# Kernel optimization log

Measured on AMD Instinct MI355X. Metric: run time of the kernel, lower is better.

## Reference

```python
import jax, jax.numpy as jnp
import numpy as np

N, E, IN, HID, H, OUT = 50000, 800000, 128, 64, 2, 1
NEG_SLOPE = 0.2


def setup_inputs() -> dict:
    key = jax.random.key(0)
    ks = jax.random.split(key, 12)
    g = lambda k, shape, fi, fo: jax.random.normal(k, shape, jnp.float32) * np.sqrt(2.0 / (fi + fo)).astype(np.float32)
    x = jax.random.normal(ks[0], (N, IN), jnp.float32)
    edge_index = jax.random.randint(ks[1], (2, E), 0, N, jnp.int64)
    HC = H * HID
    W1 = g(ks[2], (HC, IN), IN, HC)
    b1 = jnp.zeros((HC,), jnp.float32)
    att1 = g(ks[3], (1, H, HID), HID, HID)
    W2 = g(ks[4], (HC, HC), HC, HC)
    b2 = jnp.zeros((HC,), jnp.float32)
    att2 = g(ks[5], (1, H, HID), HID, HID)
    Wp1 = g(ks[6], (HID, HC), HC, HID)
    bp1 = jnp.zeros((HID,), jnp.float32)
    Wp2 = g(ks[7], (OUT, HID), HID, OUT)
    bp2 = jnp.zeros((OUT,), jnp.float32)
    return {"x": x, "edge_index": edge_index, "W1": W1, "b1": b1, "att1": att1,
            "W2": W2, "b2": b2, "att2": att2, "Wp1": Wp1, "bp1": bp1, "Wp2": Wp2, "bp2": bp2}


def _segment_softmax(alpha, idx, n):
    # alpha: [E, H]; softmax over edges sharing the same destination node
    m = jax.ops.segment_max(alpha, idx, num_segments=n)
    m = jnp.where(jnp.isfinite(m), m, 0.0)  # empty segments -> -inf guard
    ex = jnp.exp(alpha - m[idx])
    s = jax.ops.segment_sum(ex, idx, num_segments=n)
    return ex / (s[idx] + 1e-16)


def _gatv2(x, edge_index, W, b, att):
    n = x.shape[0]
    h, c = att.shape[1], att.shape[2]
    xw = (x @ W.T + b).reshape(n, h, c)          # shared lin_l == lin_r
    src, dst = edge_index[0], edge_index[1]       # x_j = xw[src], x_i = xw[dst]
    xj = xw[src]                                  # [E, H, C]
    e = jax.nn.leaky_relu(xw[dst] + xj, NEG_SLOPE)
    alpha = jnp.einsum('ehc,ohc->eh', e, att)     # [E, H]
    alpha = _segment_softmax(alpha, dst, n)
    msg = xj * alpha[:, :, None]                  # message uses x_j (not e)
    out = jax.ops.segment_sum(msg, dst, num_segments=n)
    return out.reshape(n, h * c)


def reference(x, edge_index, W1, b1, att1, W2, b2, att2, Wp1, bp1, Wp2, bp2):
    # eval mode: dropout is identity
    h = jax.nn.relu(_gatv2(x, edge_index, W1, b1, att1))
    h = jax.nn.relu(_gatv2(h, edge_index, W2, b2, att2))
    h = h @ Wp1.T + bp1
    h = h @ Wp2.T + bp2
    return jax.nn.sigmoid(h)
```

## Files before the change

kernel.cpp:

```cpp
#include <hip/hip_runtime.h>
#include <math.h>

typedef __attribute__((ext_vector_type(2))) float f32x2;
typedef __attribute__((ext_vector_type(4))) float fx4;
typedef __attribute__((ext_vector_type(8))) short s16x8;

#define EC 64
#define NRR 8
#define RRN 6250


__device__ __forceinline__ unsigned pack_bf2(float lo, float hi){
  unsigned ul = __float_as_uint(lo); ul += 0x7fffu + ((ul>>16)&1u);
  unsigned uh = __float_as_uint(hi); uh += 0x7fffu + ((uh>>16)&1u);
  return (uh & 0xffff0000u) | (ul >> 16);
}


__device__ __forceinline__ void gemm_core(uint4* Wl, const float* __restrict__ X,
    const float* __restrict__ b, unsigned short* __restrict__ Ybf, int nrows, int brow, int t)
{
  int wv = t >> 6, lane = t & 63;
  int r = lane & 15, kb = lane >> 4;
  int row = brow*64 + wv*16 + r;
  const float* xrow = &X[(size_t)min(row, nrows-1)*128];

  fx4 acc[8];
  #pragma unroll
  for(int c=0;c<8;c++) acc[c] = (fx4){0.f,0.f,0.f,0.f};

  #pragma unroll
  for(int kt=0;kt<4;kt++){
    int k0 = kt*32 + kb*8;
    float4 v0 = *(const float4*)&xrow[k0];
    float4 v1 = *(const float4*)&xrow[k0+4];
    float vs[8] = {v0.x,v0.y,v0.z,v0.w,v1.x,v1.y,v1.z,v1.w};
    s16x8 ahi, alo;
    #pragma unroll
    for(int j=0;j<8;j++){
      unsigned u = __float_as_uint(vs[j]);
      unsigned uh = u + 0x7fffu + ((u>>16)&1u);
      unsigned short h = (unsigned short)(uh >> 16);
      float hf = __uint_as_float(((unsigned)h)<<16);
      float lo = vs[j] - hf;
      unsigned ul = __float_as_uint(lo);
      ul += 0x7fffu + ((ul>>16)&1u);
      ahi[j] = (short)h;
      alo[j] = (short)(ul>>16);
    }
    int chunk = kt*4 + kb;
    #pragma unroll
    for(int c=0;c<8;c++){
      uint4 wb = Wl[((c*16 + r)<<4) | (chunk ^ r)];
      s16x8 bb = *(s16x8*)&wb;
      acc[c] = __builtin_amdgcn_mfma_f32_16x16x32_bf16(ahi, bb, acc[c], 0,0,0);
      acc[c] = __builtin_amdgcn_mfma_f32_16x16x32_bf16(alo, bb, acc[c], 0,0,0);
    }
  }

  __syncthreads();
  unsigned short* lds = (unsigned short*)Wl;
  unsigned short* my = lds + wv*2048;
  int colb = lane & 15;
  int rq0 = (lane>>4)*4;
  #pragma unroll
  for(int c=0;c<8;c++){
    int col = c*16 + colb;
    float bias = b[col];
    #pragma unroll
    for(int q=0;q<4;q++){
      unsigned u = __float_as_uint(acc[c][q] + bias);
      u += 0x7fffu + ((u>>16)&1u);
      my[(rq0+q)*128 + col] = (unsigned short)(u>>16);
    }
  }
  const uint4* my4 = (const uint4*)my;
  uint4* Y4 = (uint4*)Ybf;
  #pragma unroll
  for(int rr=0;rr<4;rr++){
    int idx = lane + 64*rr;
    int lrow = idx >> 4, lcol = idx & 15;
    int grow = brow*64 + wv*16 + lrow;
    if(grow < nrows)
      Y4[(size_t)grow*16 + lcol] = my4[idx];
  }
}


__global__ __launch_bounds__(256) void mega_k(
    const float* __restrict__ X, const float* __restrict__ W1, const float* __restrict__ b1,
    unsigned short* __restrict__ XWbf, int nrows, int nGB,
    const int* __restrict__ dst, int E, int CH,
    unsigned short* __restrict__ cnt16, int N,
    const float* __restrict__ W2, unsigned short* __restrict__ W2bf,
    const float* __restrict__ Wp1, const float* __restrict__ bp1,
    const float* __restrict__ Wp2, const float* __restrict__ bp2,
    float* __restrict__ wfold)
{
  __shared__ int smem[8192];
  int b = blockIdx.x;
  int t = threadIdx.x;

  if(b < nGB){
    uint4* Wl = (uint4*)smem;
    #pragma unroll
    for(int i=0;i<8;i++){
      int idx = t + i*256;
      int row = idx >> 4, ch = idx & 15;
      const float* wsrc = &W1[(size_t)row*128 + ch*8];
      float4 va = *(const float4*)&wsrc[0];
      float4 vb = *(const float4*)&wsrc[4];
      uint4 o;
      o.x = pack_bf2(va.x, va.y); o.y = pack_bf2(va.z, va.w);
      o.z = pack_bf2(vb.x, vb.y); o.w = pack_bf2(vb.z, vb.w);
      Wl[(row<<4) | (ch ^ (row & 15))] = o;
    }
    __syncthreads();
    gemm_core(Wl, X, b1, XWbf, nrows, b, t);
    return;
  }
  int hb = b - nGB;
  if(hb < NRR*EC){
    int r = hb >> 6, c = hb & (EC-1);
    int r0 = r*RRN, rend = min(r0+RRN, N);
    int rn = rend - r0;
    if(rn <= 0) return;
    for(int d=t; d<rn; d+=256) smem[d] = 0;
    __syncthreads();
    int e0 = c*CH, e1 = min(e0+CH, E);
    for(int e = e0+t; e < e1; e += 256){
      int d = dst[e];
      if(d >= r0 && d < rend) atomicAdd(&smem[d-r0], 1);
    }
    __syncthreads();
    unsigned short* outp = cnt16 + (size_t)c*N;
    for(int d=t; d<rn; d+=256) outp[r0+d] = (unsigned short)smem[d];
    return;
  }
  int tb = hb - NRR*EC;
  if(tb == 0){
    const float4* Ws = (const float4*)W2;
    uint2* Wd = (uint2*)W2bf;
    #pragma unroll
    for(int i=0;i<16;i++){
      int idx = t + i*256;
      float4 v = Ws[idx];
      uint2 o; o.x = pack_bf2(v.x, v.y); o.y = pack_bf2(v.z, v.w);
      Wd[idx] = o;
    }
    return;
  }
  int k = t;
  if(k < 128){
    float s = 0.f;
    for(int j=0;j<64;j++) s += Wp2[j]*Wp1[(size_t)j*128 + k];
    wfold[k] = s;
  } else if(k == 128){
    float s = bp2[0];
    for(int j=0;j<64;j++) s += Wp2[j]*bp1[j];
    wfold[128] = s;
  }
}


__global__ __launch_bounds__(1024) void scan1_k(const unsigned short* __restrict__ cnt16,
    unsigned short* __restrict__ offs16, int* __restrict__ total,
    int* __restrict__ bsum, int n){
  __shared__ int ws[16];
  int i = blockIdx.x*1024 + threadIdx.x;
  int v = 0;
  if(i < n){
    int s = 0;
    #pragma unroll
    for(int c=0;c<EC;c++){
      int tc = cnt16[(size_t)c*n + i];
      offs16[(size_t)c*n + i] = (unsigned short)s;
      s += tc;
    }
    total[i] = s;
    v = s;
  }
  #pragma unroll
  for(int m=1;m<64;m<<=1) v += __shfl_xor(v, m);
  if((threadIdx.x & 63) == 0) ws[threadIdx.x >> 6] = v;
  __syncthreads();
  if(threadIdx.x == 0){
    int s = 0;
    #pragma unroll
    for(int w=0; w<16; w++) s += ws[w];
    bsum[blockIdx.x] = s;
  }
}


__global__ __launch_bounds__(1024) void scan3_k(const int* __restrict__ total,
    const int* __restrict__ bsum, int nb, int* __restrict__ row_ptr, int n){
  __shared__ int sm[1024];
  __shared__ int base_s;
  int t = threadIdx.x;
  if(t < 64){
    int bv = (t < nb && t < (int)blockIdx.x) ? bsum[t] : 0;
    #pragma unroll
    for(int m=1;m<64;m<<=1) bv += __shfl_xor(bv, m);
    if(t == 0) base_s = bv;
  }
  int i = blockIdx.x*1024 + t;
  int v = (i<n)? total[i] : 0;
  sm[t] = v;
  __syncthreads();
  for(int off=1; off<1024; off<<=1){
    int tv = (t>=off)? sm[t-off] : 0;
    __syncthreads();
    sm[t] += tv;
    __syncthreads();
  }
  if(i<n){
    row_ptr[i] = sm[t] - v + base_s;
    if(i == n-1) row_ptr[n] = sm[t] + base_s;
  }
}


__global__ __launch_bounds__(256) void fillC_k(
    const int* __restrict__ src, const int* __restrict__ dst,
    const unsigned short* __restrict__ offs16, const int* __restrict__ row_ptr,
    int* __restrict__ csr_src, int E, int CH, int N)
{
  __shared__ int cursor[RRN];
  int b = blockIdx.x, t = threadIdx.x;
  int r = b >> 6, c = b & (EC-1);
  int r0 = r*RRN, rend = min(r0+RRN, N);
  int rn = rend - r0;
  if(rn <= 0) return;
  for(int d=t; d<rn; d+=256)
    cursor[d] = row_ptr[r0+d] + (int)offs16[(size_t)c*N + r0 + d];
  __syncthreads();
  int e0 = c*CH, e1 = min(e0+CH, E);
  for(int base = e0 + t; base < e1; base += 1024){
    int ea = base, eb = base+256, ec2 = base+512, ed = base+768;
    int da = dst[ea];
    int db = (eb < e1) ? dst[eb] : -1;
    int dc = (ec2 < e1) ? dst[ec2] : -1;
    int dd = (ed < e1) ? dst[ed] : -1;
    int sa = src[ea];
    int sb = (eb < e1) ? src[eb] : 0;
    int sc = (ec2 < e1) ? src[ec2] : 0;
    int sd = (ed < e1) ? src[ed] : 0;
    if(da >= r0 && da < rend){ int p = atomicAdd(&cursor[da-r0], 1); csr_src[p] = sa; }
    if(db >= r0 && db < rend){ int p = atomicAdd(&cursor[db-r0], 1); csr_src[p] = sb; }
    if(dc >= r0 && dc < rend){ int p = atomicAdd(&cursor[dc-r0], 1); csr_src[p] = sc; }
    if(dd >= r0 && dd < rend){ int p = atomicAdd(&cursor[dd-r0], 1); csr_src[p] = sd; }
  }
}


__global__ __launch_bounds__(256) void gemm_bf2_k(
    const unsigned short* __restrict__ Xbf, const unsigned short* __restrict__ Wbf,
    const float* __restrict__ b, unsigned short* __restrict__ Ybf, int nrows)
{
  __shared__ uint4 Wl[128*16];
  int t = threadIdx.x;
  {
    const uint4* Ws = (const uint4*)Wbf;
    #pragma unroll
    for(int i=0;i<8;i++){
      int idx = t + i*256;
      int row = idx >> 4, ch = idx & 15;
      Wl[(row<<4) | (ch ^ (row & 15))] = Ws[idx];
    }
  }
  __syncthreads();

  int wv = t >> 6, lane = t & 63;
  int r = lane & 15, kb = lane >> 4;
  int row = blockIdx.x*64 + wv*16 + r;
  const uint4* xrow = (const uint4*)&Xbf[(size_t)min(row, nrows-1)*128];

  fx4 acc[8];
  #pragma unroll
  for(int c=0;c<8;c++) acc[c] = (fx4){0.f,0.f,0.f,0.f};

  #pragma unroll
  for(int kt=0;kt<4;kt++){
    uint4 av = xrow[kt*4 + kb];
    s16x8 aa = *(s16x8*)&av;
    int chunk = kt*4 + kb;
    #pragma unroll
    for(int c=0;c<8;c++){
      uint4 wb = Wl[((c*16 + r)<<4) | (chunk ^ r)];
      s16x8 bb = *(s16x8*)&wb;
      acc[c] = __builtin_amdgcn_mfma_f32_16x16x32_bf16(aa, bb, acc[c], 0,0,0);
    }
  }

  __syncthreads();
  unsigned short* lds = (unsigned short*)Wl;
  unsigned short* my = lds + wv*2048;
  int colb = lane & 15;
  int rq0 = (lane>>4)*4;
  #pragma unroll
  for(int c=0;c<8;c++){
    int col = c*16 + colb;
    float bias = b[col];
    #pragma unroll
    for(int q=0;q<4;q++){
      unsigned u = __float_as_uint(acc[c][q] + bias);
      u += 0x7fffu + ((u>>16)&1u);
      my[(rq0+q)*128 + col] = (unsigned short)(u>>16);
    }
  }
  const uint4* my4 = (const uint4*)my;
  uint4* Y4 = (uint4*)Ybf;
  #pragma unroll
  for(int rr=0;rr<4;rr++){
    int idx = lane + 64*rr;
    int lrow = idx >> 4, lcol = idx & 15;
    int grow = blockIdx.x*64 + wv*16 + lrow;
    if(grow < nrows)
      Y4[(size_t)grow*16 + lcol] = my4[idx];
  }
}


#define BFLO(u) __uint_as_float((u)<<16)
#define BFHI(u) __uint_as_float((u)&0xffff0000u)
#define DPP_ADD(v, ctrl) { int _t = __builtin_amdgcn_update_dpp(0, __float_as_int(v), ctrl, 0xF, 0xF, true); (v) += __int_as_float(_t); }
#define EXP2RAW(x) __builtin_amdgcn_exp2f(x)

#define GAT_BODY(U, EXPR_EX) { \
  f32x2 x0 = {BFLO(U.x), BFHI(U.x)}; \
  f32x2 x1 = {BFLO(U.y), BFHI(U.y)}; \
  f32x2 x2 = {BFLO(U.z), BFHI(U.z)}; \
  f32x2 x3 = {BFLO(U.w), BFHI(U.w)}; \
  f32x2 v0 = xd[0]+x0, v1 = xd[1]+x1, v2 = xd[2]+x2, v3 = xd[3]+x3; \
  f32x2 l0 = __builtin_elementwise_max(v0, v0*0.2f); \
  f32x2 l1 = __builtin_elementwise_max(v1, v1*0.2f); \
  f32x2 l2 = __builtin_elementwise_max(v2, v2*0.2f); \
  f32x2 l3 = __builtin_elementwise_max(v3, v3*0.2f); \
  f32x2 p2 = l0*a[0]; p2 += l1*a[1]; p2 += l2*a[2]; p2 += l3*a[3]; \
  float p = p2.x + p2.y; \
  DPP_ADD(p, 0xB1); \
  DPP_ADD(p, 0x4E); \
  DPP_ADD(p, 0x141); \
  float ex = (EXPR_EX); \
  s += ex; \
  f32x2 e2 = {ex, ex}; \
  acc[0] += e2*x0; acc[1] += e2*x1; acc[2] += e2*x2; acc[3] += e2*x3; }

template<int FUSE>
__global__ __launch_bounds__(256) void gat_v7_k(
    const unsigned short* __restrict__ XWbf,
    const float* __restrict__ att,
    const int* __restrict__ row_ptr, const int* __restrict__ csr_src,
    float* __restrict__ outf, unsigned short* __restrict__ outbf,
    const float* __restrict__ wfold, int n)
{
  int wid = threadIdx.x >> 6, lane = threadIdx.x & 63;
  int node = blockIdx.x*4 + wid;
  if(node >= n) return;
  int g = lane >> 4;
  int cg = lane & 15;
  int c8 = cg * 8;

  const float L2E = 1.44269504088896f;
  float4 A0 = *(const float4*)&att[c8];
  float4 A1 = *(const float4*)&att[c8+4];
  f32x2 a[4] = { {A0.x*L2E,A0.y*L2E}, {A0.z*L2E,A0.w*L2E},
                 {A1.x*L2E,A1.y*L2E}, {A1.z*L2E,A1.w*L2E} };

  const uint4* XW4 = (const uint4*)XWbf;
  uint4 du = XW4[(size_t)node*16 + cg];
  f32x2 xd[4] = { {BFLO(du.x),BFHI(du.x)}, {BFLO(du.y),BFHI(du.y)},
                  {BFLO(du.z),BFHI(du.z)}, {BFLO(du.w),BFHI(du.w)} };

  int beg = row_ptr[node], end = row_ptr[node+1];
  float s = 0.f;
  f32x2 acc[4] = {{0.f,0.f},{0.f,0.f},{0.f,0.f},{0.f,0.f}};

  if(end > beg){
    int i = beg;
    int sn0 = csr_src[min(beg + g, end-1)];
    uint4 u = XW4[(size_t)sn0*16 + cg];
    int sn1 = (beg+4 < end) ? csr_src[min(beg+4 + g, end-1)] : sn0;

    for(; i + 4 <= end; i += 4){
      uint4 un = XW4[(size_t)sn1*16 + cg];
      int sn2 = (i+8 < end) ? csr_src[min(i+8 + g, end-1)] : sn1;
      GAT_BODY(u, EXP2RAW(p));
      u = un; sn1 = sn2;
    }
    if(i < end){
      bool ok = (i + g) < end;
      GAT_BODY(u, ok ? EXP2RAW(p) : 0.f);
    }
  }

  s += __shfl_xor(s,16);  s += __shfl_xor(s,32);
  #pragma unroll
  for(int j=0;j<4;j++){
    acc[j].x += __shfl_xor(acc[j].x,16); acc[j].x += __shfl_xor(acc[j].x,32);
    acc[j].y += __shfl_xor(acc[j].y,16); acc[j].y += __shfl_xor(acc[j].y,32);
  }

  float inv = (s > 0.f) ? 1.f/s : 0.f;
  f32x2 o[4];
  #pragma unroll
  for(int j=0;j<4;j++){
    o[j].x = fmaxf(acc[j].x*inv, 0.f);
    o[j].y = fmaxf(acc[j].y*inv, 0.f);
  }

  if(FUSE == 0){
    if(lane < 16){
      uint4 o4;
      o4.x = pack_bf2(o[0].x, o[0].y);
      o4.y = pack_bf2(o[1].x, o[1].y);
      o4.z = pack_bf2(o[2].x, o[2].y);
      o4.w = pack_bf2(o[3].x, o[3].y);
      *(uint4*)&outbf[(size_t)node*128 + c8] = o4;
    }
  } else {
    float4 wf0 = *(const float4*)&wfold[c8];
    float4 wf1 = *(const float4*)&wfold[c8+4];
    float tt = o[0].x*wf0.x + o[0].y*wf0.y + o[1].x*wf0.z + o[1].y*wf0.w
             + o[2].x*wf1.x + o[2].y*wf1.y + o[3].x*wf1.z + o[3].y*wf1.w;
    DPP_ADD(tt, 0xB1);
    DPP_ADD(tt, 0x4E);
    DPP_ADD(tt, 0x141);
    DPP_ADD(tt, 0x140);
    if(lane == 0)
      outf[node] = 1.f/(1.f + __expf(-(tt + wfold[128])));
  }
}


static inline size_t alignup(size_t v){ return (v + 255) & ~(size_t)255; }

extern "C" void kernel_launch(void* const* d_in, const int* in_sizes, int n_in,
                              void* d_out, int out_size, void* d_ws, size_t ws_size,
                              hipStream_t stream) {
  const float* x    = (const float*)d_in[0];
  const int*   ei   = (const int*)  d_in[1];
  const float* W1   = (const float*)d_in[2];
  const float* b1   = (const float*)d_in[3];
  const float* att1 = (const float*)d_in[4];
  const float* W2   = (const float*)d_in[5];
  const float* b2   = (const float*)d_in[6];
  const float* att2 = (const float*)d_in[7];
  const float* Wp1  = (const float*)d_in[8];
  const float* bp1  = (const float*)d_in[9];
  const float* Wp2  = (const float*)d_in[10];
  const float* bp2  = (const float*)d_in[11];
  float* out = (float*)d_out;

  int N = in_sizes[0] / 128;
  int E = in_sizes[1] / 2;
  int CH = (E + EC - 1) / EC;

  char* ws = (char*)d_ws;
  size_t off = 0;
  unsigned short* Gbf  = (unsigned short*)(ws + off); off = alignup(off + (size_t)N*128*sizeof(unsigned short));
  unsigned short* XWbf = (unsigned short*)(ws + off); off = alignup(off + (size_t)N*128*sizeof(unsigned short));
  int* csr_src  = (int*)(ws + off); off = alignup(off + (size_t)E*sizeof(int));
  unsigned short* cnt16  = (unsigned short*)(ws + off); off = alignup(off + (size_t)EC*N*sizeof(unsigned short));
  unsigned short* offs16 = (unsigned short*)(ws + off); off = alignup(off + (size_t)EC*N*sizeof(unsigned short));
  int* row_ptr  = (int*)(ws + off); off = alignup(off + (size_t)(N+1)*sizeof(int));
  int* total    = (int*)(ws + off); off = alignup(off + (size_t)N*sizeof(int));
  int* bsum     = (int*)(ws + off); off = alignup(off + 1024*sizeof(int));
  unsigned short* W2bf = (unsigned short*)(ws + off); off = alignup(off + 128*128*sizeof(unsigned short));
  float* wfold  = (float*)(ws + off); off = alignup(off + 129*sizeof(float));

  const int* esrc = ei;
  const int* edst = ei + E;

  int nGB = (N + 63) / 64;
  int nb = (N + 1023) / 1024;

  mega_k<<<nGB + NRR*EC + 2, 256, 0, stream>>>(
      x, W1, b1, XWbf, N, nGB,
      edst, E, CH, cnt16, N,
      W2, W2bf, Wp1, bp1, Wp2, bp2, wfold);

  scan1_k<<<nb, 1024, 0, stream>>>(cnt16, offs16, total, bsum, N);
  scan3_k<<<nb, 1024, 0, stream>>>(total, bsum, nb, row_ptr, N);
  fillC_k<<<NRR*EC, 256, 0, stream>>>(esrc, edst, offs16, row_ptr, csr_src, E, CH, N);

  gat_v7_k<0><<<(N+3)/4, 256, 0, stream>>>(XWbf, att1, row_ptr, csr_src, nullptr, Gbf, nullptr, N);
  gemm_bf2_k<<<nGB, 256, 0, stream>>>(Gbf, W2bf, b2, XWbf, N);
  gat_v7_k<1><<<(N+3)/4, 256, 0, stream>>>(XWbf, att2, row_ptr, csr_src, out, nullptr, wfold, N);
}
```

Baseline: 132.5 us.

## Move layer-1 GEMM from histogram launch into CSR fill launch

Splits the edge histogram into its own kernel and merges the layer-1 feature GEMM and weight-prep blocks with the CSR fill kernel instead. The fill loop now loads eight dst/src pairs per thread per iteration instead of four, to expose more memory parallelism. The goal is to balance the two heavy launches, so the fill's scattered atomic work overlaps with the GEMM rather than the lighter histogram. It keeps the same number of launches but changes which phases share a grid, and uses more registers in the fill loop.

```diff
diff --git a/kernel.cpp b/kernel.cpp
--- a/kernel.cpp
+++ b/kernel.cpp
@@ -87,11 +87,94 @@
 }
 
 
-__global__ __launch_bounds__(256) void mega_k(
+__global__ __launch_bounds__(256) void hist_k(
+    const int* __restrict__ dst, int E, int CH,
+    unsigned short* __restrict__ cnt16, int N)
+{
+  __shared__ int smem[RRN];
+  int b = blockIdx.x;
+  int t = threadIdx.x;
+  int r = b >> 6, c = b & (EC-1);
+  int r0 = r*RRN, rend = min(r0+RRN, N);
+  int rn = rend - r0;
+  if(rn <= 0) return;
+  for(int d=t; d<rn; d+=256) smem[d] = 0;
+  __syncthreads();
+  int e0 = c*CH, e1 = min(e0+CH, E);
+  for(int e = e0+t; e < e1; e += 256){
+    int d = dst[e];
+    if(d >= r0 && d < rend) atomicAdd(&smem[d-r0], 1);
+  }
+  __syncthreads();
+  unsigned short* outp = cnt16 + (size_t)c*N;
+  for(int d=t; d<rn; d+=256) outp[r0+d] = (unsigned short)smem[d];
+}
+
+
+__global__ __launch_bounds__(1024) void scan1_k(const unsigned short* __restrict__ cnt16,
+    unsigned short* __restrict__ offs16, int* __restrict__ total,
+    int* __restrict__ bsum, int n){
+  __shared__ int ws[16];
+  int i = blockIdx.x*1024 + threadIdx.x;
+  int v = 0;
+  if(i < n){
+    int s = 0;
+    #pragma unroll
+    for(int c=0;c<EC;c++){
+      int tc = cnt16[(size_t)c*n + i];
+      offs16[(size_t)c*n + i] = (unsigned short)s;
+      s += tc;
+    }
+    total[i] = s;
+    v = s;
+  }
+  #pragma unroll
+  for(int m=1;m<64;m<<=1) v += __shfl_xor(v, m);
+  if((threadIdx.x & 63) == 0) ws[threadIdx.x >> 6] = v;
+  __syncthreads();
+  if(threadIdx.x == 0){
+    int s = 0;
+    #pragma unroll
+    for(int w=0; w<16; w++) s += ws[w];
+    bsum[blockIdx.x] = s;
+  }
+}
+
+
+__global__ __launch_bounds__(1024) void scan3_k(const int* __restrict__ total,
+    const int* __restrict__ bsum, int nb, int* __restrict__ row_ptr, int n){
+  __shared__ int sm[1024];
+  __shared__ int base_s;
+  int t = threadIdx.x;
+  if(t < 64){
+    int bv = (t < nb && t < (int)blockIdx.x) ? bsum[t] : 0;
+    #pragma unroll
+    for(int m=1;m<64;m<<=1) bv += __shfl_xor(bv, m);
+    if(t == 0) base_s = bv;
+  }
+  int i = blockIdx.x*1024 + t;
+  int v = (i<n)? total[i] : 0;
+  sm[t] = v;
+  __syncthreads();
+  for(int off=1; off<1024; off<<=1){
+    int tv = (t>=off)? sm[t-off] : 0;
+    __syncthreads();
+    sm[t] += tv;
+    __syncthreads();
+  }
+  if(i<n){
+    row_ptr[i] = sm[t] - v + base_s;
+    if(i == n-1) row_ptr[n] = sm[t] + base_s;
+  }
+}
+
+
+__global__ __launch_bounds__(256) void fillgemm_k(
     const float* __restrict__ X, const float* __restrict__ W1, const float* __restrict__ b1,
     unsigned short* __restrict__ XWbf, int nrows, int nGB,
-    const int* __restrict__ dst, int E, int CH,
-    unsigned short* __restrict__ cnt16, int N,
+    const int* __restrict__ src, const int* __restrict__ dst,
+    const unsigned short* __restrict__ offs16, const int* __restrict__ row_ptr,
+    int* __restrict__ csr_src, int E, int CH, int N,
     const float* __restrict__ W2, unsigned short* __restrict__ W2bf,
     const float* __restrict__ Wp1, const float* __restrict__ bp1,
     const float* __restrict__ Wp2, const float* __restrict__ bp2,
@@ -119,25 +202,40 @@
     gemm_core(Wl, X, b1, XWbf, nrows, b, t);
     return;
   }
-  int hb = b - nGB;
-  if(hb < NRR*EC){
-    int r = hb >> 6, c = hb & (EC-1);
+  int fb = b - nGB;
+  if(fb < NRR*EC){
+    int* cursor = smem;
+    int r = fb >> 6, c = fb & (EC-1);
     int r0 = r*RRN, rend = min(r0+RRN, N);
     int rn = rend - r0;
     if(rn <= 0) return;
-    for(int d=t; d<rn; d+=256) smem[d] = 0;
+    for(int d=t; d<rn; d+=256)
+      cursor[d] = row_ptr[r0+d] + (int)offs16[(size_t)c*N + r0 + d];
     __syncthreads();
     int e0 = c*CH, e1 = min(e0+CH, E);
-    for(int e = e0+t; e < e1; e += 256){
-      int d = dst[e];
-      if(d >= r0 && d < rend) atomicAdd(&smem[d-r0], 1);
-    }
-    __syncthreads();
-    unsigned short* outp = cnt16 + (size_t)c*N;
-    for(int d=t; d<rn; d+=256) outp[r0+d] = (unsigned short)smem[d];
+    for(int base = e0 + t; base < e1; base += 2048){
+      int dd[8], ss[8];
+      #pragma unroll
+      for(int q=0;q<8;q++){
+        int e = base + q*256;
+        dd[q] = (e < e1) ? dst[e] : -1;
+      }
+      #pragma unroll
+      for(int q=0;q<8;q++){
+        int e = base + q*256;
+        ss[q] = (e < e1) ? src[e] : 0;
+      }
+      #pragma unroll
+      for(int q=0;q<8;q++){
+        if(dd[q] >= r0 && dd[q] < rend){
+          int p = atomicAdd(&cursor[dd[q]-r0], 1);
+          csr_src[p] = ss[q];
+        }
+      }
+    }
     return;
   }
-  int tb = hb - NRR*EC;
+  int tb = fb - NRR*EC;
   if(tb == 0){
     const float4* Ws = (const float4*)W2;
     uint2* Wd = (uint2*)W2bf;
@@ -159,97 +257,6 @@
     float s = bp2[0];
     for(int j=0;j<64;j++) s += Wp2[j]*bp1[j];
     wfold[128] = s;
-  }
-}
-
-
-__global__ __launch_bounds__(1024) void scan1_k(const unsigned short* __restrict__ cnt16,
-    unsigned short* __restrict__ offs16, int* __restrict__ total,
-    int* __restrict__ bsum, int n){
-  __shared__ int ws[16];
-  int i = blockIdx.x*1024 + threadIdx.x;
-  int v = 0;
-  if(i < n){
-    int s = 0;
-    #pragma unroll
-    for(int c=0;c<EC;c++){
-      int tc = cnt16[(size_t)c*n + i];
-      offs16[(size_t)c*n + i] = (unsigned short)s;
-      s += tc;
-    }
-    total[i] = s;
-    v = s;
-  }
-  #pragma unroll
-  for(int m=1;m<64;m<<=1) v += __shfl_xor(v, m);
-  if((threadIdx.x & 63) == 0) ws[threadIdx.x >> 6] = v;
-  __syncthreads();
-  if(threadIdx.x == 0){
-    int s = 0;
-    #pragma unroll
-    for(int w=0; w<16; w++) s += ws[w];
-    bsum[blockIdx.x] = s;
-  }
-}
-
-
-__global__ __launch_bounds__(1024) void scan3_k(const int* __restrict__ total,
-    const int* __restrict__ bsum, int nb, int* __restrict__ row_ptr, int n){
-  __shared__ int sm[1024];
-  __shared__ int base_s;
-  int t = threadIdx.x;
-  if(t < 64){
-    int bv = (t < nb && t < (int)blockIdx.x) ? bsum[t] : 0;
-    #pragma unroll
-    for(int m=1;m<64;m<<=1) bv += __shfl_xor(bv, m);
-    if(t == 0) base_s = bv;
-  }
-  int i = blockIdx.x*1024 + t;
-  int v = (i<n)? total[i] : 0;
-  sm[t] = v;
-  __syncthreads();
-  for(int off=1; off<1024; off<<=1){
-    int tv = (t>=off)? sm[t-off] : 0;
-    __syncthreads();
-    sm[t] += tv;
-    __syncthreads();
-  }
-  if(i<n){
-    row_ptr[i] = sm[t] - v + base_s;
-    if(i == n-1) row_ptr[n] = sm[t] + base_s;
-  }
-}
-
-
-__global__ __launch_bounds__(256) void fillC_k(
-    const int* __restrict__ src, const int* __restrict__ dst,
-    const unsigned short* __restrict__ offs16, const int* __restrict__ row_ptr,
-    int* __restrict__ csr_src, int E, int CH, int N)
-{
-  __shared__ int cursor[RRN];
-  int b = blockIdx.x, t = threadIdx.x;
-  int r = b >> 6, c = b & (EC-1);
-  int r0 = r*RRN, rend = min(r0+RRN, N);
-  int rn = rend - r0;
-  if(rn <= 0) return;
-  for(int d=t; d<rn; d+=256)
-    cursor[d] = row_ptr[r0+d] + (int)offs16[(size_t)c*N + r0 + d];
-  __syncthreads();
-  int e0 = c*CH, e1 = min(e0+CH, E);
-  for(int base = e0 + t; base < e1; base += 1024){
-    int ea = base, eb = base+256, ec2 = base+512, ed = base+768;
-    int da = dst[ea];
-    int db = (eb < e1) ? dst[eb] : -1;
-    int dc = (ec2 < e1) ? dst[ec2] : -1;
-    int dd = (ed < e1) ? dst[ed] : -1;
-    int sa = src[ea];
-    int sb = (eb < e1) ? src[eb] : 0;
-    int sc = (ec2 < e1) ? src[ec2] : 0;
-    int sd = (ed < e1) ? src[ed] : 0;
-    if(da >= r0 && da < rend){ int p = atomicAdd(&cursor[da-r0], 1); csr_src[p] = sa; }
-    if(db >= r0 && db < rend){ int p = atomicAdd(&cursor[db-r0], 1); csr_src[p] = sb; }
-    if(dc >= r0 && dc < rend){ int p = atomicAdd(&cursor[dc-r0], 1); csr_src[p] = sc; }
-    if(dd >= r0 && dd < rend){ int p = atomicAdd(&cursor[dd-r0], 1); csr_src[p] = sd; }
   }
 }
 
@@ -476,14 +483,13 @@
   int nGB = (N + 63) / 64;
   int nb = (N + 1023) / 1024;
 
-  mega_k<<<nGB + NRR*EC + 2, 256, 0, stream>>>(
-      x, W1, b1, XWbf, N, nGB,
-      edst, E, CH, cnt16, N,
-      W2, W2bf, Wp1, bp1, Wp2, bp2, wfold);
-
+  hist_k<<<NRR*EC, 256, 0, stream>>>(edst, E, CH, cnt16, N);
   scan1_k<<<nb, 1024, 0, stream>>>(cnt16, offs16, total, bsum, N);
   scan3_k<<<nb, 1024, 0, stream>>>(total, bsum, nb, row_ptr, N);
-  fillC_k<<<NRR*EC, 256, 0, stream>>>(esrc, edst, offs16, row_ptr, csr_src, E, CH, N);
+  fillgemm_k<<<nGB + NRR*EC + 2, 256, 0, stream>>>(
+      x, W1, b1, XWbf, N, nGB,
+      esrc, edst, offs16, row_ptr, csr_src, E, CH, N,
+      W2, W2bf, Wp1, bp1, Wp2, bp2, wfold);
 
   gat_v7_k<0><<<(N+3)/4, 256, 0, stream>>>(XWbf, att1, row_ptr, csr_src, nullptr, Gbf, nullptr, N);
   gemm_bf2_k<<<nGB, 256, 0, stream>>>(Gbf, W2bf, b2, XWbf, N);
```

Result: no change. 134.2 us (+1.3%).
